# Optimization experiments

Measured on AMD Instinct MI355X. Metric: run time of the kernel, lower is better.

Reference implementation:

```python
import math
import jax, jax.numpy as jnp
import numpy as np

B, H, T, D = 4, 16, 1024, 64


def setup_inputs() -> dict:
    key0 = jax.random.key(0)
    ks = jax.random.split(key0, 5)
    return {
        "query": jax.random.normal(ks[0], (B, H, T, D), dtype=jnp.float32),
        "key": jax.random.normal(ks[1], (B, H, T, D), dtype=jnp.float32),
        "value": jax.random.normal(ks[2], (B, H, T, D), dtype=jnp.float32),
        "edges_key": jax.random.normal(ks[3], (T, T, D), dtype=jnp.float32),
        "edges_value": jax.random.normal(ks[4], (T, T, D), dtype=jnp.float32),
        "mask": jnp.ones((B, 1, 1, T), dtype=bool),
    }


def reference(query, key, value, edges_key, edges_value, mask):
    d = query.shape[-1]
    # content-content scores [B,H,T,T]
    scores = jnp.einsum("bhqd,bhkd->bhqk", query, key)
    # content-position scores via relative edge keys [T,T,D]
    scores = scores + jnp.einsum("bhqd,qkd->bhqk", query, edges_key)
    scores = scores * (1.0 / math.sqrt(d))
    scores = jnp.where(mask, scores, jnp.float32(-1e9))
    a = jax.nn.softmax(scores, axis=-1)  # dropout is identity in eval / pdrop=0
    # value update + relative edge-value update
    out = jnp.einsum("bhqk,bhkd->bhqd", a, value)
    out = out + jnp.einsum("bhqk,qkd->bhqd", a, edges_value)
    return out
```

## Files before the change

### kernel.cpp

```cpp
#include <hip/hip_runtime.h>

#define Tt 1024
#define Dh 64
#define BHn 64
#define SCALE 0.125f

typedef __attribute__((ext_vector_type(4))) float f32x4;
typedef __attribute__((ext_vector_type(8))) short bf16x8;

__device__ inline unsigned short f2bf(float x){
  unsigned u = __float_as_uint(x);
  unsigned r = (u + 0x7FFFu + ((u >> 16) & 1u)) >> 16;
  return (unsigned short)r;
}
__device__ inline float bf2f(unsigned short h){
  return __uint_as_float(((unsigned)h) << 16);
}
__device__ inline ushort4 pack4(float4 f){
  ushort4 u; u.x=f2bf(f.x); u.y=f2bf(f.y); u.z=f2bf(f.z); u.w=f2bf(f.w); return u;
}
__device__ inline bf16x8 pack8(float4 a, float4 b){
  bf16x8 r;
  r[0]=(short)f2bf(a.x); r[1]=(short)f2bf(a.y); r[2]=(short)f2bf(a.z); r[3]=(short)f2bf(a.w);
  r[4]=(short)f2bf(b.x); r[5]=(short)f2bf(b.y); r[6]=(short)f2bf(b.z); r[7]=(short)f2bf(b.w);
  return r;
}
__device__ inline f32x4 mfma16(bf16x8 a, bf16x8 b, f32x4 c){
  return __builtin_amdgcn_mfma_f32_16x16x32_bf16(a, b, c, 0, 0, 0);
}

__device__ inline void stage64x64(const float* __restrict__ g, unsigned short (*lds)[68], int tid){
  int r = tid >> 2, c = (tid & 3) * 16;
  const float4* g4 = (const float4*)(g + (size_t)r * 64 + c);
  float4 f0 = g4[0], f1 = g4[1], f2_ = g4[2], f3 = g4[3];
  ushort4* d4 = (ushort4*)&lds[r][c];
  d4[0]=pack4(f0); d4[1]=pack4(f1); d4[2]=pack4(f2_); d4[3]=pack4(f3);
}
__device__ inline void stage64x64T(const float* __restrict__ g, unsigned short (*lds)[68], int tid){
  int r = tid >> 2, c = (tid & 3) * 16;
  const float4* g4 = (const float4*)(g + (size_t)r * 64 + c);
  float4 f[4] = { g4[0], g4[1], g4[2], g4[3] };
#pragma unroll
  for (int i = 0; i < 4; ++i){
    lds[c + 4*i + 0][r] = f2bf(f[i].x);
    lds[c + 4*i + 1][r] = f2bf(f[i].y);
    lds[c + 4*i + 2][r] = f2bf(f[i].z);
    lds[c + 4*i + 3][r] = f2bf(f[i].w);
  }
}
__device__ inline void stage_rows(const unsigned short* __restrict__ g, size_t rowstride,
                                  unsigned short (*lds)[68], int tid){
  int r = tid >> 2, c = (tid & 3) * 16;
  const ushort4* s4 = (const ushort4*)(g + (size_t)r * rowstride + c);
  ushort4 u0=s4[0], u1=s4[1], u2=s4[2], u3=s4[3];
  ushort4* d4 = (ushort4*)&lds[r][c];
  d4[0]=u0; d4[1]=u1; d4[2]=u2; d4[3]=u3;
}
__device__ inline bf16x8 ldsfrag(const unsigned short (*lds)[68], int row, int col){
  const ushort4* p = (const ushort4*)&lds[row][col];
  ushort4 u0 = p[0], u1 = p[1];
  bf16x8 r;
  r[0]=(short)u0.x; r[1]=(short)u0.y; r[2]=(short)u0.z; r[3]=(short)u0.w;
  r[4]=(short)u1.x; r[5]=(short)u1.y; r[6]=(short)u1.z; r[7]=(short)u1.w;
  return r;
}
__device__ inline float fragsum(bf16x8 v){
  float s = 0.f;
#pragma unroll
  for (int i = 0; i < 8; ++i) s += bf2f((unsigned short)v[i]);
  return s;
}

__global__ __launch_bounds__(256) void k_qek(const float* __restrict__ Q,
                                             const float* __restrict__ EK,
                                             unsigned short* __restrict__ BIAS){
  __shared__ unsigned short ek[64][68];
  __shared__ unsigned short ot[64][68];
  const int qi = blockIdx.x;
  const int tid = threadIdx.x;
  const int w = tid >> 6, l = tid & 63, lr = l & 15, lg = l >> 4;

  bf16x8 a0, a1;
  {
    const int bh = 16*w + lr;
    const float4* q4 = (const float4*)(Q + ((size_t)bh * Tt + qi) * Dh);
    a0 = pack8(q4[lg*2],     q4[lg*2 + 1]);
    a1 = pack8(q4[8 + lg*2], q4[8 + lg*2 + 1]);
  }

  for (int kt = 0; kt < 16; ++kt){
    stage64x64(EK + ((size_t)qi * Tt + kt*64) * Dh, ek, tid);
    __syncthreads();
    f32x4 acc[4];
#pragma unroll
    for (int c = 0; c < 4; ++c){
      bf16x8 b0 = ldsfrag(ek, c*16 + lr, lg*8);
      bf16x8 b1 = ldsfrag(ek, c*16 + lr, lg*8 + 32);
      f32x4 z = {0.f,0.f,0.f,0.f};
      z = mfma16(a0, b0, z);
      z = mfma16(a1, b1, z);
      acc[c] = z;
    }
#pragma unroll
    for (int c = 0; c < 4; ++c)
#pragma unroll
      for (int j = 0; j < 4; ++j)
        ot[16*w + lg*4 + j][c*16 + lr] = f2bf(acc[c][j]);
    __syncthreads();
    {
      int r = tid >> 2, c2 = (tid & 3) * 16;
      unsigned short* dst = BIAS + (size_t)r * Tt * Tt + (size_t)qi * Tt + kt*64 + c2;
      const ushort4* s4 = (const ushort4*)&ot[r][c2];
      ushort4 u0=s4[0], u1=s4[1], u2=s4[2], u3=s4[3];
      ushort4* d4 = (ushort4*)dst;
      d4[0]=u0; d4[1]=u1; d4[2]=u2; d4[3]=u3;
    }
    __syncthreads();
  }
}

__global__ __launch_bounds__(256) void k_attn(const float* __restrict__ Q,
                                              const float* __restrict__ K,
                                              const float* __restrict__ V,
                                              unsigned short* __restrict__ WS,
                                              float* __restrict__ OUT){
  __shared__ unsigned short kt_[64][68];
  __shared__ unsigned short bt[64][68];
  __shared__ unsigned short pt[64][68];
  __shared__ unsigned short vt[64][68];
  const int qt = blockIdx.x * 64;
  const int bh = blockIdx.y;
  const int tid = threadIdx.x;
  const int w = tid >> 6, l = tid & 63, lr = l & 15, lg = l >> 4;

  bf16x8 a0, a1;
  {
    const float4* q4 = (const float4*)(Q + ((size_t)bh * Tt + qt + 16*w + lr) * Dh);
    a0 = pack8(q4[lg*2],     q4[lg*2 + 1]);
    a1 = pack8(q4[8 + lg*2], q4[8 + lg*2 + 1]);
  }

  float lsum[4] = {0.f, 0.f, 0.f, 0.f};
  f32x4 oacc[4];
#pragma unroll
  for (int c = 0; c < 4; ++c) oacc[c] = (f32x4){0.f,0.f,0.f,0.f};

  for (int kt = 0; kt < 16; ++kt){
    stage64x64(K + ((size_t)bh * Tt + kt*64) * Dh, kt_, tid);
    stage_rows(WS + (size_t)bh * Tt * Tt + (size_t)qt * Tt + kt*64, Tt, bt, tid);
    stage64x64T(V + ((size_t)bh * Tt + kt*64) * Dh, vt, tid);
    __syncthreads();
#pragma unroll
    for (int c = 0; c < 4; ++c){
      bf16x8 b0 = ldsfrag(kt_, c*16 + lr, lg*8);
      bf16x8 b1 = ldsfrag(kt_, c*16 + lr, lg*8 + 32);
      f32x4 z = {0.f,0.f,0.f,0.f};
      z = mfma16(a0, b0, z);
      z = mfma16(a1, b1, z);
      int kl = c*16 + lr;
#pragma unroll
      for (int j = 0; j < 4; ++j){
        float s = (z[j] + bf2f(bt[16*w + lg*4 + j][kl])) * SCALE;
        float p = __expf(s);
        lsum[j] += p;
        pt[16*w + lg*4 + j][kl] = f2bf(p);
      }
    }
    __syncthreads();
    {
      int r = tid >> 2, c2 = (tid & 3) * 16;
      unsigned short* dst = WS + (size_t)bh * Tt * Tt + (size_t)(qt + r) * Tt + kt*64 + c2;
      const ushort4* s4 = (const ushort4*)&pt[r][c2];
      ushort4 u0=s4[0], u1=s4[1], u2=s4[2], u3=s4[3];
      ushort4* d4 = (ushort4*)dst;
      d4[0]=u0; d4[1]=u1; d4[2]=u2; d4[3]=u3;
    }
    bf16x8 p0 = ldsfrag(pt, 16*w + lr, lg*8);
    bf16x8 p1 = ldsfrag(pt, 16*w + lr, lg*8 + 32);
#pragma unroll
    for (int c = 0; c < 4; ++c){
      bf16x8 v0 = ldsfrag(vt, c*16 + lr, lg*8);
      bf16x8 v1 = ldsfrag(vt, c*16 + lr, lg*8 + 32);
      oacc[c] = mfma16(p0, v0, oacc[c]);
      oacc[c] = mfma16(p1, v1, oacc[c]);
    }
    __syncthreads();
  }
  float rl[4];
#pragma unroll
  for (int j = 0; j < 4; ++j){
    float su = lsum[j];
    for (int o = 1; o < 16; o <<= 1) su += __shfl_xor(su, o, 64);
    rl[j] = 1.f / su;
  }
#pragma unroll
  for (int c = 0; c < 4; ++c)
#pragma unroll
    for (int j = 0; j < 4; ++j){
      int qrow = qt + 16*w + lg*4 + j;
      OUT[((size_t)bh * Tt + qrow) * Dh + c*16 + lr] = oacc[c][j] * rl[j];
    }
}

__global__ __launch_bounds__(256) void k_aev(const unsigned short* __restrict__ WS,
                                             const float* __restrict__ EV,
                                             float* __restrict__ OUT){
  __shared__ unsigned short at[64][68];
  __shared__ unsigned short evt[64][68];
  __shared__ float sums[64];
  const int qi = blockIdx.x;
  const int tid = threadIdx.x;
  const int w = tid >> 6, l = tid & 63, lr = l & 15, lg = l >> 4;

  f32x4 acc[4];
#pragma unroll
  for (int c = 0; c < 4; ++c) acc[c] = (f32x4){0.f,0.f,0.f,0.f};
  float asum = 0.f;

  for (int kt = 0; kt < 16; ++kt){
    stage_rows(WS + (size_t)qi * Tt + kt*64, (size_t)Tt * Tt, at, tid);
    stage64x64T(EV + ((size_t)qi * Tt + kt*64) * Dh, evt, tid);
    __syncthreads();
    bf16x8 a0 = ldsfrag(at, 16*w + lr, lg*8);
    bf16x8 a1 = ldsfrag(at, 16*w + lr, lg*8 + 32);
    asum += fragsum(a0) + fragsum(a1);
#pragma unroll
    for (int c = 0; c < 4; ++c){
      bf16x8 b0 = ldsfrag(evt, c*16 + lr, lg*8);
      bf16x8 b1 = ldsfrag(evt, c*16 + lr, lg*8 + 32);
      acc[c] = mfma16(a0, b0, acc[c]);
      acc[c] = mfma16(a1, b1, acc[c]);
    }
    __syncthreads();
  }
  asum += __shfl_xor(asum, 16, 64);
  asum += __shfl_xor(asum, 32, 64);
  if (lg == 0) sums[16*w + lr] = asum;
  __syncthreads();

#pragma unroll
  for (int c = 0; c < 4; ++c)
#pragma unroll
    for (int j = 0; j < 4; ++j){
      int bh = 16*w + lg*4 + j;
      float rl = 1.f / sums[bh];
      size_t idx = ((size_t)bh * Tt + qi) * Dh + c*16 + lr;
      OUT[idx] += acc[c][j] * rl;
    }
}

extern "C" void kernel_launch(void* const* d_in, const int* in_sizes, int n_in,
                              void* d_out, int out_size, void* d_ws, size_t ws_size,
                              hipStream_t stream){
  const float* Q  = (const float*)d_in[0];
  const float* K  = (const float*)d_in[1];
  const float* V  = (const float*)d_in[2];
  const float* EK = (const float*)d_in[3];
  const float* EV = (const float*)d_in[4];
  float* OUT = (float*)d_out;
  unsigned short* WS = (unsigned short*)d_ws;

  if (ws_size < (size_t)BHn * Tt * Tt * sizeof(unsigned short)) return;

  k_qek <<<dim3(1024),    dim3(256), 0, stream>>>(Q, EK, WS);
  k_attn<<<dim3(16, 64),  dim3(256), 0, stream>>>(Q, K, V, WS, OUT);
  k_aev <<<dim3(1024),    dim3(256), 0, stream>>>(WS, EV, OUT);
}
```

Baseline: 279.9 us.

## Double-buffer edge tiles, use per-wave staging, and remap attention block order

k_qek and k_aev now double-buffer the per-query edge tiles in shared memory, so the next tile loads while the current one is computed. Several block-wide barriers are replaced with wave barriers over per-wave staging buffers. k_aev reads probability fragments straight from global memory instead of staging them through LDS. k_attn uses a 1D grid with a swizzled (bh, q-tile) mapping meant to improve cache locality. Dropping the restrict qualifier on WS and using wave barriers in place of block barriers carries some correctness risk.

```diff
diff --git a/kernel.cpp b/kernel.cpp
--- a/kernel.cpp
+++ b/kernel.cpp
@@ -2,7 +2,6 @@
 
 #define Tt 1024
 #define Dh 64
-#define BHn 64
 #define SCALE 0.125f
 
 typedef __attribute__((ext_vector_type(4))) float f32x4;
@@ -74,28 +73,33 @@
 __global__ __launch_bounds__(256) void k_qek(const float* __restrict__ Q,
                                              const float* __restrict__ EK,
                                              unsigned short* __restrict__ BIAS){
-  __shared__ unsigned short ek[64][68];
-  __shared__ unsigned short ot[64][68];
+  __shared__ unsigned short ek[2][64][68];
+  __shared__ unsigned short ot[4][16][68];
   const int qi = blockIdx.x;
   const int tid = threadIdx.x;
   const int w = tid >> 6, l = tid & 63, lr = l & 15, lg = l >> 4;
 
   bf16x8 a0, a1;
   {
-    const int bh = 16*w + lr;
-    const float4* q4 = (const float4*)(Q + ((size_t)bh * Tt + qi) * Dh);
+    const float4* q4 = (const float4*)(Q + ((size_t)(16*w + lr) * Tt + qi) * Dh);
     a0 = pack8(q4[lg*2],     q4[lg*2 + 1]);
     a1 = pack8(q4[8 + lg*2], q4[8 + lg*2 + 1]);
   }
+  const float* ekq = EK + (size_t)qi * Tt * Dh;
+  const int r = l >> 2, c2 = (l & 3) * 16;
+  unsigned short* dst0 = BIAS + (size_t)(16*w + r) * Tt * Tt + (size_t)qi * Tt + c2;
+
+  stage64x64(ekq, ek[0], tid);
+  __syncthreads();
 
   for (int kt = 0; kt < 16; ++kt){
-    stage64x64(EK + ((size_t)qi * Tt + kt*64) * Dh, ek, tid);
-    __syncthreads();
+    if (kt < 15) stage64x64(ekq + (size_t)(kt+1) * 64 * Dh, ek[(kt+1)&1], tid);
+    const unsigned short (*cur)[68] = ek[kt&1];
     f32x4 acc[4];
 #pragma unroll
     for (int c = 0; c < 4; ++c){
-      bf16x8 b0 = ldsfrag(ek, c*16 + lr, lg*8);
-      bf16x8 b1 = ldsfrag(ek, c*16 + lr, lg*8 + 32);
+      bf16x8 b0 = ldsfrag(cur, c*16 + lr, lg*8);
+      bf16x8 b1 = ldsfrag(cur, c*16 + lr, lg*8 + 32);
       f32x4 z = {0.f,0.f,0.f,0.f};
       z = mfma16(a0, b0, z);
       z = mfma16(a1, b1, z);
@@ -105,16 +109,15 @@
     for (int c = 0; c < 4; ++c)
 #pragma unroll
       for (int j = 0; j < 4; ++j)
-        ot[16*w + lg*4 + j][c*16 + lr] = f2bf(acc[c][j]);
-    __syncthreads();
+        ot[w][lg*4 + j][c*16 + lr] = f2bf(acc[c][j]);
+    __builtin_amdgcn_wave_barrier();
     {
-      int r = tid >> 2, c2 = (tid & 3) * 16;
-      unsigned short* dst = BIAS + (size_t)r * Tt * Tt + (size_t)qi * Tt + kt*64 + c2;
-      const ushort4* s4 = (const ushort4*)&ot[r][c2];
+      const ushort4* s4 = (const ushort4*)&ot[w][r][c2];
       ushort4 u0=s4[0], u1=s4[1], u2=s4[2], u3=s4[3];
-      ushort4* d4 = (ushort4*)dst;
+      ushort4* d4 = (ushort4*)(dst0 + kt*64);
       d4[0]=u0; d4[1]=u1; d4[2]=u2; d4[3]=u3;
     }
+    __builtin_amdgcn_wave_barrier();
     __syncthreads();
   }
 }
@@ -122,14 +125,15 @@
 __global__ __launch_bounds__(256) void k_attn(const float* __restrict__ Q,
                                               const float* __restrict__ K,
                                               const float* __restrict__ V,
-                                              unsigned short* __restrict__ WS,
+                                              unsigned short* WS,
                                               float* __restrict__ OUT){
   __shared__ unsigned short kt_[64][68];
   __shared__ unsigned short bt[64][68];
   __shared__ unsigned short pt[64][68];
   __shared__ unsigned short vt[64][68];
-  const int qt = blockIdx.x * 64;
-  const int bh = blockIdx.y;
+  const int bid = blockIdx.x;
+  const int bh = (bid & 7) + ((bid >> 7) << 3);
+  const int qt = ((bid >> 3) & 15) * 64;
   const int tid = threadIdx.x;
   const int w = tid >> 6, l = tid & 63, lr = l & 15, lg = l >> 4;
 
@@ -139,16 +143,19 @@
     a0 = pack8(q4[lg*2],     q4[lg*2 + 1]);
     a1 = pack8(q4[8 + lg*2], q4[8 + lg*2 + 1]);
   }
-
-  float lsum[4] = {0.f, 0.f, 0.f, 0.f};
+  const float* kb = K + (size_t)bh * Tt * Dh;
+  const float* vb = V + (size_t)bh * Tt * Dh;
+  unsigned short* wsb = WS + (size_t)bh * Tt * Tt;
+
+  float lsum[4] = {0.f,0.f,0.f,0.f};
   f32x4 oacc[4];
 #pragma unroll
   for (int c = 0; c < 4; ++c) oacc[c] = (f32x4){0.f,0.f,0.f,0.f};
 
   for (int kt = 0; kt < 16; ++kt){
-    stage64x64(K + ((size_t)bh * Tt + kt*64) * Dh, kt_, tid);
-    stage_rows(WS + (size_t)bh * Tt * Tt + (size_t)qt * Tt + kt*64, Tt, bt, tid);
-    stage64x64T(V + ((size_t)bh * Tt + kt*64) * Dh, vt, tid);
+    stage64x64(kb + (size_t)kt * 64 * Dh, kt_, tid);
+    stage_rows(wsb + (size_t)qt * Tt + kt*64, Tt, bt, tid);
+    stage64x64T(vb + (size_t)kt * 64 * Dh, vt, tid);
     __syncthreads();
 #pragma unroll
     for (int c = 0; c < 4; ++c){
@@ -169,10 +176,9 @@
     __syncthreads();
     {
       int r = tid >> 2, c2 = (tid & 3) * 16;
-      unsigned short* dst = WS + (size_t)bh * Tt * Tt + (size_t)(qt + r) * Tt + kt*64 + c2;
       const ushort4* s4 = (const ushort4*)&pt[r][c2];
       ushort4 u0=s4[0], u1=s4[1], u2=s4[2], u3=s4[3];
-      ushort4* d4 = (ushort4*)dst;
+      ushort4* d4 = (ushort4*)(wsb + (size_t)(qt + r) * Tt + kt*64 + c2);
       d4[0]=u0; d4[1]=u1; d4[2]=u2; d4[3]=u3;
     }
     bf16x8 p0 = ldsfrag(pt, 16*w + lr, lg*8);
@@ -196,38 +202,40 @@
 #pragma unroll
   for (int c = 0; c < 4; ++c)
 #pragma unroll
-    for (int j = 0; j < 4; ++j){
-      int qrow = qt + 16*w + lg*4 + j;
-      OUT[((size_t)bh * Tt + qrow) * Dh + c*16 + lr] = oacc[c][j] * rl[j];
-    }
+    for (int j = 0; j < 4; ++j)
+      OUT[((size_t)bh * Tt + qt + 16*w + lg*4 + j) * Dh + c*16 + lr] = oacc[c][j] * rl[j];
 }
 
 __global__ __launch_bounds__(256) void k_aev(const unsigned short* __restrict__ WS,
                                              const float* __restrict__ EV,
                                              float* __restrict__ OUT){
-  __shared__ unsigned short at[64][68];
-  __shared__ unsigned short evt[64][68];
+  __shared__ unsigned short evt[2][64][68];
   __shared__ float sums[64];
   const int qi = blockIdx.x;
   const int tid = threadIdx.x;
   const int w = tid >> 6, l = tid & 63, lr = l & 15, lg = l >> 4;
 
+  const unsigned short* arow = WS + (size_t)(16*w + lr) * Tt * Tt + (size_t)qi * Tt;
+  const float* evq = EV + (size_t)qi * Tt * Dh;
+
   f32x4 acc[4];
 #pragma unroll
   for (int c = 0; c < 4; ++c) acc[c] = (f32x4){0.f,0.f,0.f,0.f};
   float asum = 0.f;
 
+  stage64x64T(evq, evt[0], tid);
+  __syncthreads();
+
   for (int kt = 0; kt < 16; ++kt){
-    stage_rows(WS + (size_t)qi * Tt + kt*64, (size_t)Tt * Tt, at, tid);
-    stage64x64T(EV + ((size_t)qi * Tt + kt*64) * Dh, evt, tid);
-    __syncthreads();
-    bf16x8 a0 = ldsfrag(at, 16*w + lr, lg*8);
-    bf16x8 a1 = ldsfrag(at, 16*w + lr, lg*8 + 32);
+    if (kt < 15) stage64x64T(evq + (size_t)(kt+1) * 64 * Dh, evt[(kt+1)&1], tid);
+    const unsigned short (*cur)[68] = evt[kt&1];
+    bf16x8 a0 = *(const bf16x8*)(arow + kt*64 + lg*8);
+    bf16x8 a1 = *(const bf16x8*)(arow + kt*64 + 32 + lg*8);
     asum += fragsum(a0) + fragsum(a1);
 #pragma unroll
     for (int c = 0; c < 4; ++c){
-      bf16x8 b0 = ldsfrag(evt, c*16 + lr, lg*8);
-      bf16x8 b1 = ldsfrag(evt, c*16 + lr, lg*8 + 32);
+      bf16x8 b0 = ldsfrag(cur, c*16 + lr, lg*8);
+      bf16x8 b1 = ldsfrag(cur, c*16 + lr, lg*8 + 32);
       acc[c] = mfma16(a0, b0, acc[c]);
       acc[c] = mfma16(a1, b1, acc[c]);
     }
@@ -236,7 +244,7 @@
   asum += __shfl_xor(asum, 16, 64);
   asum += __shfl_xor(asum, 32, 64);
   if (lg == 0) sums[16*w + lr] = asum;
-  __syncthreads();
+  __builtin_amdgcn_wave_barrier();
 
 #pragma unroll
   for (int c = 0; c < 4; ++c)
@@ -260,9 +268,9 @@
   float* OUT = (float*)d_out;
   unsigned short* WS = (unsigned short*)d_ws;
 
-  if (ws_size < (size_t)BHn * Tt * Tt * sizeof(unsigned short)) return;
-
-  k_qek <<<dim3(1024),    dim3(256), 0, stream>>>(Q, EK, WS);
-  k_attn<<<dim3(16, 64),  dim3(256), 0, stream>>>(Q, K, V, WS, OUT);
-  k_aev <<<dim3(1024),    dim3(256), 0, stream>>>(WS, EV, OUT);
-}
+  if (ws_size < (size_t)64 * Tt * Tt * sizeof(unsigned short)) return;
+
+  k_qek <<<dim3(1024), dim3(256), 0, stream>>>(Q, EK, WS);
+  k_attn<<<dim3(1024), dim3(256), 0, stream>>>(Q, K, V, WS, OUT);
+  k_aev <<<dim3(1024), dim3(256), 0, stream>>>(WS, EV, OUT);
+}
```

Measured after the change: 272.6 us. 1.03x faster.
